# Kernel optimization log

Hardware: AMD Instinct MI355X
Metric: run time of the kernel (lower is better)

## Reference

```python
import jax, jax.numpy as jnp
import numpy as np

T_LEN, BATCH, IN_SIZE, HID = 512, 64, 1024, 1024
EPS = 1e-6


def layer_norm(x, alpha, beta, eps=EPS):
    # Matches torch: mean over last dim, UNBIASED variance (ddof=1)
    mu = jnp.mean(x, axis=-1, keepdims=True)
    var = jnp.var(x, axis=-1, keepdims=True, ddof=1)
    xn = (x - mu) / jnp.sqrt(var + eps)
    return alpha * xn + beta


def setup_inputs() -> dict:
    key = jax.random.key(0)
    ks = jax.random.split(key, 12)
    std = 1.0 / np.sqrt(HID)
    u = lambda k, shape: jax.random.uniform(k, shape, jnp.float32, -std, std)
    return {
        "x": jax.random.normal(ks[0], (T_LEN, BATCH, IN_SIZE), jnp.float32),
        "Wi": u(ks[1], (4 * HID, IN_SIZE)),
        "bi": u(ks[2], (4 * HID,)),
        "Wh": u(ks[3], (4 * HID, HID)),
        "bh": u(ks[4], (4 * HID,)),
        "g_i2h": u(ks[5], (4 * HID,)),
        "b_i2h": u(ks[6], (4 * HID,)),
        "g_h2h": u(ks[7], (4 * HID,)),
        "b_h2h": u(ks[8], (4 * HID,)),
        "g_cell": u(ks[9], (HID,)),
        "b_cell": u(ks[10], (HID,)),
    }


def reference(x, Wi, bi, Wh, bh, g_i2h, b_i2h, g_h2h, b_h2h, g_cell, b_cell):
    # Faithful to the source: h and c are NEVER updated inside the loop
    # (the original code omits h = h_t / c = c_t), so every timestep sees
    # the initial zero state -> fully parallel over time.
    T, B, _ = x.shape
    H = Wh.shape[1]
    h0 = jnp.zeros((B, H), x.dtype)
    c0 = jnp.zeros((B, H), x.dtype)

    i2h = layer_norm(jnp.einsum('tbi,gi->tbg', x, Wi) + bi, g_i2h, b_i2h)  # [T,B,4H]
    h2h = layer_norm(h0 @ Wh.T + bh, g_h2h, b_h2h)                          # [B,4H]
    preact = i2h + h2h                                                      # [T,B,4H]

    gates = jax.nn.sigmoid(preact[..., :3 * H])
    g_t = jnp.tanh(preact[..., 3 * H:])
    f_t = gates[..., H:2 * H]
    o_t = gates[..., 2 * H:3 * H]
    # i_t = gates[..., :H] is computed in the original but unused

    c_t = c0 * f_t + (1.0 - f_t) * g_t
    c_t = layer_norm(c_t, g_cell, b_cell)
    h_t = o_t * jnp.tanh(c_t)  # [T,B,H]

    return h_t, h_t[-1]
```

## Files before the change

### kernel.cpp

```cpp
#include <hip/hip_runtime.h>
#include <hip/hip_bf16.h>
#include <stdint.h>


#define MROWS 32768L
#define NCOLS 4096
#define KDIM  1024

typedef __bf16 bf16x8 __attribute__((ext_vector_type(8)));
typedef __bf16 bf16x4 __attribute__((ext_vector_type(4)));
typedef float  f32x4  __attribute__((ext_vector_type(4)));

__device__ float g_Cvec[4096];

__device__ __forceinline__ void gload16(char* lds, const char* g) {
  __builtin_amdgcn_global_load_lds(
      (const __attribute__((address_space(1))) char*)g,
      (__attribute__((address_space(3))) char*)lds, 16, 0, 0);
}

__device__ __forceinline__ void block_reduce2(float& a, float& b, float* red, int tid) {
#pragma unroll
  for (int m = 32; m > 0; m >>= 1) {
    a += __shfl_xor(a, m, 64);
    b += __shfl_xor(b, m, 64);
  }
  const int lane = tid & 63, wid = tid >> 6;
  if (lane == 0) { red[wid] = a; red[4 + wid] = b; }
  __syncthreads();
  a = red[0] + red[1] + red[2] + red[3];
  b = red[4] + red[5] + red[6] + red[7];
  __syncthreads();
}

__global__ __launch_bounds__(256) void cast_kernel(const float4* __restrict__ in,
                                                   bf16x4* __restrict__ out, int n4) {
  int i = blockIdx.x * 256 + threadIdx.x;
  const int stride = gridDim.x * 256;
  for (; i < n4; i += stride) {
    const float4 v = in[i];
    bf16x4 o = { (__bf16)v.x, (__bf16)v.y, (__bf16)v.z, (__bf16)v.w };
    out[i] = o;
  }
}

__global__ __launch_bounds__(256) void prep_kernel(const float* __restrict__ bh,
                                                   const float* __restrict__ b_i2h,
                                                   const float* __restrict__ g_h2h,
                                                   const float* __restrict__ b_h2h) {
  __shared__ float red[8];
  const int tid = threadIdx.x;
  float v[16];
  float s = 0.f, ss = 0.f;
#pragma unroll
  for (int u = 0; u < 16; ++u) {
    v[u] = bh[tid + u * 256];
    s += v[u]; ss += v[u] * v[u];
  }
  block_reduce2(s, ss, red, tid);
  const float mu  = s * (1.f / 4096.f);
  const float var = (ss - 4096.f * mu * mu) * (1.f / 4095.f);
  const float rs  = rsqrtf(var + 1e-6f);
#pragma unroll
  for (int u = 0; u < 16; ++u) {
    const int g = tid + u * 256;
    g_Cvec[g] = b_i2h[g] + g_h2h[g] * ((v[u] - mu) * rs) + b_h2h[g];
  }
}


#define LGKM0() do { asm volatile("s_waitcnt lgkmcnt(0)" ::: "memory"); \
    __builtin_amdgcn_sched_barrier(0); } while (0)
#define BAR()   __builtin_amdgcn_s_barrier()
#define VMCNT(n) asm volatile("s_waitcnt vmcnt(" #n ")" ::: "memory")

#define STG_A(s, h) { char* d_ = Al + (((s) & 1) << 15) + ((h) << 14); \
    const char* g_ = Ag + (long)(h) * 262144 + (s) * 128; \
    gload16(d_, g_); gload16(d_ + 8192, g_ + 131072); }

#define STG_B(s, h) { char* d_ = Bl + (((s) & 1) << 15) + ((h) << 14); \
    const char* g_ = Bg + (long)(h) * 262144 + (s) * 128; \
    gload16(d_, g_); gload16(d_ + 8192, g_ + 131072); }

#define ABASE(t) ((const char*)As + (((t) & 1) << 15) + (wr << 14))
#define BBASE(t) ((const char*)Bs + (((t) & 1) << 15) + ((wc >> 1) << 14))

#define RD_Ax(arr, Ahalf, c) { _Pragma("unroll") for (int mi_ = 0; mi_ < 4; ++mi_) { \
    const char* p_ = (Ahalf) + (((c) * 64 + mi_ * 16 + fr) << 7); \
    arr[mi_][0] = *(const bf16x8*)(p_ + cb0); \
    arr[mi_][1] = *(const bf16x8*)(p_ + cb1); } }

#define RD_Bx(arr, Bhalf, g) { _Pragma("unroll") for (int nj_ = 0; nj_ < 2; ++nj_) { \
    const char* p_ = (Bhalf) + ((brow0 + (g) * 32 + nj_ * 16 + fr) << 7); \
    arr[nj_][0] = *(const bf16x8*)(p_ + cb0); \
    arr[nj_][1] = *(const bf16x8*)(p_ + cb1); } }

#define MMQ(X, Y, c, g) { _Pragma("unroll") for (int mi_ = 0; mi_ < 4; ++mi_) { \
    _Pragma("unroll") for (int nj_ = 0; nj_ < 2; ++nj_) { \
      acc[(c)*4+mi_][(g)*2+nj_] = __builtin_amdgcn_mfma_f32_16x16x32_bf16( \
          X[mi_][0], Y[nj_][0], acc[(c)*4+mi_][(g)*2+nj_], 0, 0, 0); \
      acc[(c)*4+mi_][(g)*2+nj_] = __builtin_amdgcn_mfma_f32_16x16x32_bf16( \
          X[mi_][1], Y[nj_][1], acc[(c)*4+mi_][(g)*2+nj_], 0, 0, 0); } } }

#define SETP1() __builtin_amdgcn_s_setprio(1)
#define SETP0() __builtin_amdgcn_s_setprio(0)

#define TILE(t, Ac, An, Bc, Bn, G1, G2) { \
    const char* AhC = ABASE(t); const char* BhC = BBASE(t); \
    const char* AhN = ABASE((t) + 1); const char* BhN = BBASE((t) + 1); \
     LGKM0(); RD_Ax(An, AhC, 1); if (G1) STG_B((t) + 1, 1); \
    SETP1(); MMQ(Ac, Bc, 0, 0); SETP0(); BAR(); \
     LGKM0(); RD_Bx(Bn, BhC, 1); \
    SETP1(); MMQ(An, Bc, 1, 0); SETP0(); BAR(); \
     LGKM0(); if (G2) STG_A((t) + 2, 0); \
    SETP1(); MMQ(An, Bn, 1, 1); SETP0(); \
    if (G2) { VMCNT(2); } else { VMCNT(0); } BAR(); \
     if (G1) { RD_Ax(An, AhN, 0); RD_Bx(Bc, BhN, 0); } \
    if (G2) { STG_A((t) + 2, 1); STG_B((t) + 2, 0); } \
    SETP1(); MMQ(Ac, Bn, 0, 1); SETP0(); BAR(); }

__global__ __launch_bounds__(512, 2) void gemm_kernel(const __bf16* __restrict__ A,
                                                      const __bf16* __restrict__ B,
                                                      __bf16* __restrict__ Y, long r0) {
  __shared__ __align__(16) __bf16 As[2 * 2 * 8192];
  __shared__ __align__(16) __bf16 Bs[2 * 2 * 8192];

  const int tid  = threadIdx.x;
  const int lane = tid & 63;
  const int wid  = tid >> 6;
  const int wr   = wid >> 2;
  const int wc   = wid & 3;

  const int nwg = gridDim.x;
  const int q8 = nwg >> 3, r8 = nwg & 7;
  const int xcd = blockIdx.x & 7, rest = blockIdx.x >> 3;
  const int wgid = (xcd < r8 ? xcd * (q8 + 1) : r8 * (q8 + 1) + (xcd - r8) * q8) + rest;
  const long m0 = (long)(wgid >> 4) * 256;
  const long n0 = (long)(wgid & 15) * 256;

  const int scol = (((tid & 7) ^ ((tid >> 3) & 7)) << 4);
  const char* Ag = (const char*)(A + (r0 + m0) * KDIM) + (long)(tid >> 3) * 2048 + scol;
  const char* Bg = (const char*)(B + n0 * KDIM) + (long)(tid >> 3) * 2048 + scol;
  char* Al = (char*)As + tid * 16;
  char* Bl = (char*)Bs + tid * 16;

  const int fr  = lane & 15;
  const int sw  = (fr & 7) << 4;
  const int cb0 = (((lane >> 4) << 4)) ^ sw;
  const int cb1 = (64 | ((lane >> 4) << 4)) ^ sw;
  const int brow0 = (wc & 1) << 6;

  f32x4 acc[8][4];
  const f32x4 z = {0.f, 0.f, 0.f, 0.f};
#pragma unroll
  for (int i = 0; i < 8; ++i)
#pragma unroll
    for (int j = 0; j < 4; ++j) acc[i][j] = z;

  bf16x8 A0[4][2], A1[4][2], B0[2][2], B1[2][2];

  STG_A(0, 0); STG_A(0, 1); STG_B(0, 0); STG_B(0, 1);
  STG_A(1, 0); STG_A(1, 1); STG_B(1, 0);
  VMCNT(6);
  BAR();
  RD_Ax(A0, ABASE(0), 0); RD_Bx(B0, BBASE(0), 0);

#pragma unroll 1
  for (int tt = 0; tt < 7; ++tt) {
    const int t = tt * 2;
    TILE(t,     A0, A1, B0, B1, true, true);
    TILE(t + 1, A1, A0, B0, B1, true, true);
  }
  TILE(14, A0, A1, B0, B1, true,  false);
  TILE(15, A1, A0, B0, B1, false, false);

  const long mrow = m0 + wr * 128 + ((lane >> 4) << 2);
  const long ncol = n0 + wc * 64 + fr;
  __bf16* Yp = Y + mrow * NCOLS + ncol;
#pragma unroll
  for (int c = 0; c < 2; ++c)
#pragma unroll
    for (int mi = 0; mi < 4; ++mi)
#pragma unroll
      for (int nj = 0; nj < 4; ++nj)
#pragma unroll
        for (int r = 0; r < 4; ++r)
          Yp[(long)(c * 64 + mi * 16 + r) * NCOLS + nj * 16] = (__bf16)acc[c * 4 + mi][nj][r];
}

__global__ __launch_bounds__(256) void pass2_kernel(const __bf16* __restrict__ Yw,
                                                    const float* __restrict__ bi,
                                                    const float* __restrict__ g_i2h,
                                                    const float* __restrict__ g_cell,
                                                    const float* __restrict__ b_cell,
                                                    float* __restrict__ out, long r0) {
  __shared__ float p0[4096];
  __shared__ float red[8];
  const int tid  = threadIdx.x;
  const long row = r0 + blockIdx.x;
  const bf16x8* yv = (const bf16x8*)(Yw + (long)blockIdx.x * NCOLS);

  float s = 0.f, ss = 0.f;
#pragma unroll
  for (int it = 0; it < 2; ++it) {
    const int ch = tid + it * 256;
    const bf16x8 v = yv[ch];
    const float4 b0 = ((const float4*)bi)[ch * 2];
    const float4 b1 = ((const float4*)bi)[ch * 2 + 1];
    float p[8];
    p[0] = (float)v[0] + b0.x;  p[1] = (float)v[1] + b0.y;
    p[2] = (float)v[2] + b0.z;  p[3] = (float)v[3] + b0.w;
    p[4] = (float)v[4] + b1.x;  p[5] = (float)v[5] + b1.y;
    p[6] = (float)v[6] + b1.z;  p[7] = (float)v[7] + b1.w;
#pragma unroll
    for (int u = 0; u < 8; ++u) {
      p0[ch * 8 + u] = p[u];
      s += p[u];
      ss += p[u] * p[u];
    }
  }
  block_reduce2(s, ss, red, tid);
  const float mu  = s * (1.f / 4096.f);
  const float var = (ss - 4096.f * mu * mu) * (1.f / 4095.f);
  const float rs  = rsqrtf(var + 1e-6f);

  float cc[4], oo[4];
  float s2 = 0.f, ss2 = 0.f;
#pragma unroll
  for (int u = 0; u < 4; ++u) {
    const int j = tid + u * 256;
    const float pf = g_i2h[1024 + j] * ((p0[1024 + j] - mu) * rs) + g_Cvec[1024 + j];
    const float po = g_i2h[2048 + j] * ((p0[2048 + j] - mu) * rs) + g_Cvec[2048 + j];
    const float pg = g_i2h[3072 + j] * ((p0[3072 + j] - mu) * rs) + g_Cvec[3072 + j];
    const float f  = 1.f / (1.f + __expf(-pf));
    oo[u] = 1.f / (1.f + __expf(-po));
    const float e2 = __expf(2.f * pg);
    const float gt = (e2 - 1.f) / (e2 + 1.f);
    cc[u] = (1.f - f) * gt;
    s2 += cc[u]; ss2 += cc[u] * cc[u];
  }
  block_reduce2(s2, ss2, red, tid);
  const float mu2  = s2 * (1.f / 1024.f);
  const float var2 = (ss2 - 1024.f * mu2 * mu2) * (1.f / 1023.f);
  const float rs2  = rsqrtf(var2 + 1e-6f);

  const long obase = row * 1024;
#pragma unroll
  for (int u = 0; u < 4; ++u) {
    const int j = tid + u * 256;
    const float cn = g_cell[j] * ((cc[u] - mu2) * rs2) + b_cell[j];
    const float e2 = __expf(2.f * cn);
    const float th = (e2 - 1.f) / (e2 + 1.f);
    const float h  = oo[u] * th;
    out[obase + j] = h;
    if (row >= MROWS - 64)
      out[MROWS * 1024 + ((row - (MROWS - 64)) << 10) + j] = h;
  }
}

extern "C" void kernel_launch(void* const* d_in, const int* in_sizes, int n_in,
                              void* d_out, int out_size, void* d_ws, size_t ws_size,
                              hipStream_t stream) {
  (void)in_sizes; (void)n_in; (void)out_size;
  const float* x      = (const float*)d_in[0];
  const float* Wi     = (const float*)d_in[1];
  const float* bi     = (const float*)d_in[2];
  const float* bh     = (const float*)d_in[4];
  const float* g_i2h  = (const float*)d_in[5];
  const float* b_i2h  = (const float*)d_in[6];
  const float* g_h2h  = (const float*)d_in[7];
  const float* b_h2h  = (const float*)d_in[8];
  const float* g_cell = (const float*)d_in[9];
  const float* b_cell = (const float*)d_in[10];
  float* out = (float*)d_out;

  __bf16* xb = (__bf16*)d_ws;
  __bf16* wb = (__bf16*)((char*)d_ws + 67108864);
  __bf16* y  = (__bf16*)((char*)d_ws + 75497472);

  cast_kernel<<<2048, 256, 0, stream>>>((const float4*)x, (bf16x4*)xb, 33554432 / 4);
  cast_kernel<<<1024, 256, 0, stream>>>((const float4*)Wi, (bf16x4*)wb, 4194304 / 4);
  prep_kernel<<<1, 256, 0, stream>>>(bh, b_i2h, g_h2h, b_h2h);

  long avail = (long)ws_size - 75497472L;
  long max_rows = (avail / (NCOLS * 2)) & ~255L;
  if (max_rows > 8192) max_rows = 8192;
  if (max_rows < 256)  max_rows = 256;
  for (long rbase = 0; rbase < MROWS; rbase += max_rows) {
    const long rows = (MROWS - rbase < max_rows) ? (MROWS - rbase) : max_rows;
    gemm_kernel<<<dim3((rows / 256) * 16), 512, 0, stream>>>(xb, wb, y, rbase);
    pass2_kernel<<<dim3(rows), 256, 0, stream>>>(y, bi, g_i2h, g_cell, b_cell, out, rbase);
  }
}
```

Before: 428.4 us.

## Restructure GEMM main loop into eight-phase schedule with interleaved LDS reads and staging

Replaces the four-phase TILE macro, which prefetched the next fragments into alternate registers, with a TWOTILE macro that runs eight phases per pair of K-tiles. Each phase issues LDS fragment reads and a global-to-LDS stage, then synchronizes with barriers and an lgkmcnt wait before its MFMA block. The aim is to spread global loads and LDS reads more evenly across MFMA bursts and drop the register double-buffering. The cost is more barriers per tile and less overlap between LDS reads and MFMAs, because reads are now awaited right before use.

```diff
diff --git a/kernel.cpp b/kernel.cpp
--- a/kernel.cpp
+++ b/kernel.cpp
@@ -71,8 +71,11 @@
 
 #define LGKM0() do { asm volatile("s_waitcnt lgkmcnt(0)" ::: "memory"); \
     __builtin_amdgcn_sched_barrier(0); } while (0)
+#define LGKM8() asm volatile("s_waitcnt lgkmcnt(8)" ::: "memory")
 #define BAR()   __builtin_amdgcn_s_barrier()
 #define VMCNT(n) asm volatile("s_waitcnt vmcnt(" #n ")" ::: "memory")
+#define SETP1() __builtin_amdgcn_s_setprio(1)
+#define SETP0() __builtin_amdgcn_s_setprio(0)
 
 #define STG_A(s, h) { char* d_ = Al + (((s) & 1) << 15) + ((h) << 14); \
     const char* g_ = Ag + (long)(h) * 262144 + (s) * 128; \
@@ -102,22 +105,25 @@
       acc[(c)*4+mi_][(g)*2+nj_] = __builtin_amdgcn_mfma_f32_16x16x32_bf16( \
           X[mi_][1], Y[nj_][1], acc[(c)*4+mi_][(g)*2+nj_], 0, 0, 0); } } }
 
-#define SETP1() __builtin_amdgcn_s_setprio(1)
-#define SETP0() __builtin_amdgcn_s_setprio(0)
-
-#define TILE(t, Ac, An, Bc, Bn, G1, G2) { \
-    const char* AhC = ABASE(t); const char* BhC = BBASE(t); \
-    const char* AhN = ABASE((t) + 1); const char* BhN = BBASE((t) + 1); \
-     LGKM0(); RD_Ax(An, AhC, 1); if (G1) STG_B((t) + 1, 1); \
-    SETP1(); MMQ(Ac, Bc, 0, 0); SETP0(); BAR(); \
-     LGKM0(); RD_Bx(Bn, BhC, 1); \
-    SETP1(); MMQ(An, Bc, 1, 0); SETP0(); BAR(); \
-     LGKM0(); if (G2) STG_A((t) + 2, 0); \
-    SETP1(); MMQ(An, Bn, 1, 1); SETP0(); \
-    if (G2) { VMCNT(2); } else { VMCNT(0); } BAR(); \
-     if (G1) { RD_Ax(An, AhN, 0); RD_Bx(Bc, BhN, 0); } \
-    if (G2) { STG_A((t) + 2, 1); STG_B((t) + 2, 0); } \
-    SETP1(); MMQ(Ac, Bn, 0, 1); SETP0(); BAR(); }
+#define TWOTILE(t, S0, S1, S2, VMA, VMB) { \
+    const char* At_ = ABASE(t); const char* Bt_ = BBASE(t); \
+    const char* Au_ = ABASE((t) + 1); const char* Bu_ = BBASE((t) + 1); \
+     RD_Ax(A0, At_, 0); RD_Bx(B01, Bt_, 0); if (S0) STG_B((t) + 1, 1); \
+           LGKM8(); BAR(); LGKM0(); SETP1(); MMQ(A0, B01, 0, 0); SETP0(); BAR(); \
+     RD_Ax(A1, At_, 1); if (S1) STG_A((t) + 2, 0); \
+           BAR(); LGKM0(); SETP1(); MMQ(A1, B01, 1, 0); SETP0(); BAR(); \
+     RD_Bx(B23, Bt_, 1); if (S1) STG_A((t) + 2, 1); \
+           BAR(); LGKM0(); SETP1(); MMQ(A1, B23, 1, 1); SETP0(); BAR(); \
+     if (S1) STG_B((t) + 2, 0); VMA; \
+           BAR(); LGKM0(); SETP1(); MMQ(A0, B23, 0, 1); SETP0(); BAR(); \
+     RD_Ax(A0, Au_, 0); RD_Bx(B01, Bu_, 0); if (S1) STG_B((t) + 2, 1); \
+           LGKM8(); BAR(); LGKM0(); SETP1(); MMQ(A0, B01, 0, 0); SETP0(); BAR(); \
+     RD_Ax(A1, Au_, 1); if (S2) STG_A((t) + 3, 0); \
+           BAR(); LGKM0(); SETP1(); MMQ(A1, B01, 1, 0); SETP0(); BAR(); \
+     RD_Bx(B23, Bu_, 1); if (S2) STG_A((t) + 3, 1); \
+           BAR(); LGKM0(); SETP1(); MMQ(A1, B23, 1, 1); SETP0(); BAR(); \
+     if (S2) STG_B((t) + 3, 0); VMB; \
+           BAR(); LGKM0(); SETP1(); MMQ(A0, B23, 0, 1); SETP0(); BAR(); }
 
 __global__ __launch_bounds__(512, 2) void gemm_kernel(const __bf16* __restrict__ A,
                                                       const __bf16* __restrict__ B,
@@ -157,22 +163,19 @@
 #pragma unroll
     for (int j = 0; j < 4; ++j) acc[i][j] = z;
 
-  bf16x8 A0[4][2], A1[4][2], B0[2][2], B1[2][2];
+  bf16x8 A0[4][2], A1[4][2], B01[2][2], B23[2][2];
 
   STG_A(0, 0); STG_A(0, 1); STG_B(0, 0); STG_B(0, 1);
   STG_A(1, 0); STG_A(1, 1); STG_B(1, 0);
   VMCNT(6);
   BAR();
-  RD_Ax(A0, ABASE(0), 0); RD_Bx(B0, BBASE(0), 0);
 
 #pragma unroll 1
   for (int tt = 0; tt < 7; ++tt) {
     const int t = tt * 2;
-    TILE(t,     A0, A1, B0, B1, true, true);
-    TILE(t + 1, A1, A0, B0, B1, true, true);
-  }
-  TILE(14, A0, A1, B0, B1, true,  false);
-  TILE(15, A1, A0, B0, B1, false, false);
+    TWOTILE(t, true, true, true, VMCNT(6), VMCNT(6));
+  }
+  TWOTILE(14, true, false, false, VMCNT(0), ((void)0));
 
   const long mrow = m0 + wr * 128 + ((lane >> 4) << 2);
   const long ncol = n0 + wc * 64 + fr;
```

New measurement: 438.2 us. 1.02x slower.
